# Optimization experiments

Hardware: AMD Instinct MI355X
Metric: run time of the kernel (lower is better)

## Reference

```python
import jax, jax.numpy as jnp
import numpy as np

N = 50000   # nodes
E = 800000  # edges (avg degree 16)
D = 128     # input = hidden = embedding dim
K1 = 25000  # ceil(0.5 * N)
K2 = 12500  # ceil(0.5 * K1)
LABELS = 5
BN_EPS = 1e-5


def _sage(x, src, dst, W, b, normalize):
    # old-PyG SAGEConv: remove self loops, add self loop, mean aggregate, linear, L2-normalize
    n = x.shape[0]
    dst_e = jnp.where(src == dst, n, dst)  # drop self loops; dummy edges (src=dst=n) also land in segment n
    s = jax.ops.segment_sum(x[src], dst_e, num_segments=n + 1)[:n]          # [n, d]
    deg = jax.ops.segment_sum(jnp.ones(src.shape, x.dtype), dst_e, num_segments=n + 1)[:n]
    agg = (s + x) / (deg + 1.0)[:, None]  # mean over neighbors + self
    out = agg @ W + b
    if normalize:
        out = out / jnp.maximum(jnp.linalg.norm(out, axis=-1, keepdims=True), 1e-12)
    return out


def _bn(x, g, b):
    # training-mode BatchNorm1d over nodes (biased variance, like torch)
    m = x.mean(axis=0)
    v = jnp.var(x, axis=0)
    return (x - m) / jnp.sqrt(v + BN_EPS) * g + b


def _sag_pool(x, src, dst, wp, bp, k):
    # SAGPooling: score = tanh(SAGEConv(x)->1), global top_k (single graph), filter_adj via dummy remap
    n = x.shape[0]
    score = jnp.tanh(_sage(x, src, dst, wp[:, None], bp, normalize=False)[:, 0])  # [n]
    score_k, perm = jax.lax.top_k(score, k)
    x2 = x[perm] * score_k[:, None]
    rank = jnp.full((n + 1,), -1, jnp.int32).at[perm].set(jnp.arange(k, dtype=jnp.int32))
    rs, rd = rank[src], rank[dst]
    valid = (rs >= 0) & (rd >= 0)
    src2 = jnp.where(valid, rs, k)  # invalid edges -> dummy node k
    dst2 = jnp.where(valid, rd, k)
    return x2, src2, dst2


def _forward(x, edge_index, Wc, bc, gamma, beta, Wpool, bpool, W1, b1, W2, b2):
    src, dst = edge_index[0], edge_index[1]
    # source bug replicated: stage 3 layer 2 uses bn_3_1's params
    bn_idx = [[0, 1, 2], [3, 4, 5], [6, 6, 8]]
    ks = [K1, K2]
    outs = []
    for s in range(3):
        for i in range(3):
            li = 3 * s + i
            x = jax.nn.relu(_sage(x, src, dst, Wc[li], bc[li], True))
            bi = bn_idx[s][i]
            x = _bn(x, gamma[bi], beta[bi])
        outs.append(jnp.max(x, axis=0))  # scatter_max with a single graph
        if s < 2:
            x, src, dst = _sag_pool(x, src, dst, Wpool[s], bpool[s], ks[s])
    h = jnp.concatenate(outs)[None, :]          # [1, 3*D]
    h = jax.nn.relu(h @ W1 + b1)
    return h @ W2 + b2                           # [1, LABELS]


def setup_inputs() -> dict:
    key = jax.random.key(0)
    ks = jax.random.split(key, 8)
    x = jax.random.normal(ks[0], (N, D), dtype=jnp.float32)
    edge_index = jax.random.randint(ks[1], (2, E), 0, N, dtype=jnp.int32)
    Wc = jax.random.normal(ks[2], (9, D, D), dtype=jnp.float32) / np.sqrt(D)
    bc = jnp.zeros((9, D), jnp.float32)
    gamma = jnp.ones((9, D), jnp.float32)
    beta = jnp.zeros((9, D), jnp.float32)
    Wpool = jax.random.normal(ks[3], (2, D), dtype=jnp.float32) / np.sqrt(D)
    bpool = jnp.zeros((2,), jnp.float32)
    W1 = jax.random.normal(ks[4], (3 * D, 50), dtype=jnp.float32) / np.sqrt(3 * D)
    b1 = jnp.zeros((50,), jnp.float32)
    W2 = jax.random.normal(ks[5], (50, LABELS), dtype=jnp.float32) / np.sqrt(50)
    b2 = jnp.zeros((LABELS,), jnp.float32)
    return {"x": x, "edge_index": edge_index, "Wc": Wc, "bc": bc, "gamma": gamma,
            "beta": beta, "Wpool": Wpool, "bpool": bpool,
            "W1": W1, "b1": b1, "W2": W2, "b2": b2}


def reference(x, edge_index, Wc, bc, gamma, beta, Wpool, bpool, W1, b1, W2, b2):
    return _forward(x, edge_index, Wc, bc, gamma, beta, Wpool, bpool, W1, b1, W2, b2)
```

## Files before the change

kernel.cpp:

```cpp
#include <hip/hip_runtime.h>

constexpr int FD   = 128;
constexpr int NMAX = 50000;
constexpr int EDG  = 800000;

static __device__ __forceinline__ unsigned enc(float f){
  unsigned u = __float_as_uint(f);
  return (u & 0x80000000u) ? ~u : (u | 0x80000000u);
}
static __device__ __forceinline__ float dec(unsigned e){
  unsigned u = (e & 0x80000000u) ? (e ^ 0x80000000u) : ~e;
  return __uint_as_float(u);
}

__global__ void k_count(const int* __restrict__ src, const int* __restrict__ dst,
                        int* __restrict__ deg, int E){
  int e = blockIdx.x*256 + threadIdx.x;
  if (e >= E) return;
  int s = src[e], d = dst[e];
  if (s != d) atomicAdd(&deg[d], 1);
}

__global__ void k_remap_count(const int* __restrict__ sIn, const int* __restrict__ dIn,
                              int* __restrict__ sOut, int* __restrict__ dOut,
                              const int* __restrict__ rank, int kNew,
                              int* __restrict__ deg, int E){
  int e = blockIdx.x*256 + threadIdx.x;
  if (e >= E) return;
  int s = sIn[e], d = dIn[e];
  int rs = rank[s], rd = rank[d];
  bool ok = (rs >= 0) && (rd >= 0);
  int os = ok ? rs : kNew, od = ok ? rd : kNew;
  sOut[e] = os; dOut[e] = od;
  if (os != od) atomicAdd(&deg[od], 1);
}

__global__ void k_scan(int* __restrict__ off, int* __restrict__ cur, int n){
  __shared__ int wsum[16];
  __shared__ int carry;
  int tid = threadIdx.x, lane = tid & 63, wid = tid >> 6;
  if (tid == 0) carry = 0;
  __syncthreads();
  for (int base = 0; base < n; base += 1024){
    int v = base + tid;
    int x = (v < n) ? off[v] : 0;
    int val = x;
    #pragma unroll
    for (int o = 1; o < 64; o <<= 1){ int t = __shfl_up(val, o); if (lane >= o) val += t; }
    if (lane == 63) wsum[wid] = val;
    __syncthreads();
    if (tid < 16){
      int v2 = wsum[tid];
      #pragma unroll
      for (int o = 1; o < 16; o <<= 1){ int t = __shfl_up(v2, o); if (tid >= o) v2 += t; }
      wsum[tid] = v2;
    }
    __syncthreads();
    int add = (wid > 0) ? wsum[wid-1] : 0;
    int incl = val + add;
    int c0 = carry;
    if (v < n){ int e0 = c0 + incl - x; off[v] = e0; cur[v] = e0; }
    __syncthreads();
    if (tid == 0) carry = c0 + wsum[15];
    __syncthreads();
  }
  if (tid == 0) off[n] = carry;
}

__global__ void k_fill(const int* __restrict__ src, const int* __restrict__ dst,
                       int* __restrict__ cur, int* __restrict__ csr, int E){
  int e = blockIdx.x*256 + threadIdx.x;
  if (e >= E) return;
  int s = src[e], d = dst[e];
  if (s != d){ int pos = atomicAdd(&cur[d], 1); csr[pos] = s; }
}

__global__ __launch_bounds__(256) void k_agg(const float* __restrict__ X,
    const int* __restrict__ off, const int* __restrict__ csr,
    float* __restrict__ AGG, int n,
    const float* __restrict__ st, const float* __restrict__ g,
    const float* __restrict__ bt, float invn){
  int tid = threadIdx.x;
  int v = blockIdx.x*4 + (tid >> 6);
  if (v >= n) return;
  int lane = tid & 63;
  int c = lane * 2;
  float ax = 1.f, ay = 1.f, bx = 0.f, by = 0.f;
  if (st){
    float ma = st[c]*invn, mb = st[c+1]*invn;
    float va = st[FD+c]*invn - ma*ma, vb = st[FD+c+1]*invn - mb*mb;
    ax = g[c]*rsqrtf(va + 1e-5f);  ay = g[c+1]*rsqrtf(vb + 1e-5f);
    bx = bt[c] - ma*ax;            by = bt[c+1] - mb*ay;
  }
  int b = off[v], e = off[v+1];
  int deg = e - b;
  float2 s = *(const float2*)(X + (size_t)v*FD + c);
  int j = 0;
  while (j < deg){
    int cnt = deg - j; if (cnt > 64) cnt = 64;
    int myu = (j + lane < deg) ? csr[b + j + lane] : 0;
    int t = 0;
    for (; t + 4 <= cnt; t += 4){
      int u0 = __shfl(myu, t);
      int u1 = __shfl(myu, t+1);
      int u2 = __shfl(myu, t+2);
      int u3 = __shfl(myu, t+3);
      float2 t0 = *(const float2*)(X + (size_t)u0*FD + c);
      float2 t1 = *(const float2*)(X + (size_t)u1*FD + c);
      float2 t2 = *(const float2*)(X + (size_t)u2*FD + c);
      float2 t3 = *(const float2*)(X + (size_t)u3*FD + c);
      s.x += t0.x + t1.x + t2.x + t3.x;
      s.y += t0.y + t1.y + t2.y + t3.y;
    }
    for (; t < cnt; t++){
      int u = __shfl(myu, t);
      float2 tt = *(const float2*)(X + (size_t)u*FD + c);
      s.x += tt.x; s.y += tt.y;
    }
    j += cnt;
  }
  float inv = 1.f / (float)(deg + 1);
  float2 o;
  o.x = s.x*inv*ax + bx;
  o.y = s.y*inv*ay + by;
  *(float2*)(AGG + (size_t)v*FD + c) = o;
}

__global__ __launch_bounds__(256,2) void k_gemm(const float* __restrict__ A,
    const float* __restrict__ W, const float* __restrict__ bias,
    float* __restrict__ Y, float* __restrict__ stats, int n,
    unsigned* __restrict__ cmx, unsigned* __restrict__ cmn){
  __shared__ float sW[FD*FD];
  __shared__ float ss[4][FD];
  __shared__ float sq_[4][FD];
  __shared__ float smx[4][FD];
  __shared__ float smn[4][FD];
  int tid = threadIdx.x;
  {
    const float4* Wg = (const float4*)W; float4* Ws = (float4*)sW;
    for (int i = tid; i < FD*FD/4; i += 256) Ws[i] = Wg[i];
  }
  __syncthreads();
  int tc = tid & 15;
  int tr = tid >> 4;
  int rbase = blockIdx.x*FD + tr*8;
  float acc[8][8];
  #pragma unroll
  for (int i = 0; i < 8; i++)
    #pragma unroll
    for (int j = 0; j < 8; j++) acc[i][j] = 0.f;

  for (int k4 = 0; k4 < FD; k4 += 4){
    float4 a[8];
    #pragma unroll
    for (int i = 0; i < 8; i++){
      int r = rbase + i; if (r >= n) r = n - 1;
      a[i] = *(const float4*)(A + (size_t)r*FD + k4);
    }
    #pragma unroll
    for (int kk = 0; kk < 4; kk++){
      const float* wr = &sW[(k4+kk)*FD + tc*8];
      float4 w0 = *(const float4*)wr, w1 = *(const float4*)(wr+4);
      #pragma unroll
      for (int i = 0; i < 8; i++){
        float av = (kk==0) ? a[i].x : (kk==1) ? a[i].y : (kk==2) ? a[i].z : a[i].w;
        acc[i][0] += av*w0.x; acc[i][1] += av*w0.y; acc[i][2] += av*w0.z; acc[i][3] += av*w0.w;
        acc[i][4] += av*w1.x; acc[i][5] += av*w1.y; acc[i][6] += av*w1.z; acc[i][7] += av*w1.w;
      }
    }
  }
  float bx[8];
  {
    const float* bp = bias + tc*8;
    #pragma unroll
    for (int j = 0; j < 8; j++) bx[j] = bp[j];
  }
  float cs[8], cq[8], mxv[8], mnv[8];
  #pragma unroll
  for (int j = 0; j < 8; j++){ cs[j]=0.f; cq[j]=0.f; mxv[j]=-3.4e38f; mnv[j]=3.4e38f; }
  #pragma unroll
  for (int i = 0; i < 8; i++){
    int r = rbase + i;
    bool valid = (r < n);
    float y[8]; float sq = 0.f;
    #pragma unroll
    for (int j = 0; j < 8; j++){ y[j] = acc[i][j] + bx[j]; sq += y[j]*y[j]; }
    sq += __shfl_xor(sq,1); sq += __shfl_xor(sq,2); sq += __shfl_xor(sq,4); sq += __shfl_xor(sq,8);
    float nrm = sqrtf(sq);
    float sc = 1.f / fmaxf(nrm, 1e-12f);
    #pragma unroll
    for (int j = 0; j < 8; j++){ y[j] *= sc; y[j] = fmaxf(y[j], 0.f); }
    if (valid){
      float* yo = Y + (size_t)r*FD + tc*8;
      *(float4*)yo     = make_float4(y[0],y[1],y[2],y[3]);
      *(float4*)(yo+4) = make_float4(y[4],y[5],y[6],y[7]);
      #pragma unroll
      for (int j = 0; j < 8; j++){
        cs[j] += y[j]; cq[j] += y[j]*y[j];
        mxv[j] = fmaxf(mxv[j], y[j]); mnv[j] = fminf(mnv[j], y[j]);
      }
    }
  }
  #pragma unroll
  for (int j = 0; j < 8; j++){
    cs[j] += __shfl_xor(cs[j],16); cs[j] += __shfl_xor(cs[j],32);
    cq[j] += __shfl_xor(cq[j],16); cq[j] += __shfl_xor(cq[j],32);
    mxv[j] = fmaxf(mxv[j], __shfl_xor(mxv[j],16)); mxv[j] = fmaxf(mxv[j], __shfl_xor(mxv[j],32));
    mnv[j] = fminf(mnv[j], __shfl_xor(mnv[j],16)); mnv[j] = fminf(mnv[j], __shfl_xor(mnv[j],32));
  }
  int wv = tid >> 6, lane = tid & 63;
  if (lane < 16){
    #pragma unroll
    for (int j = 0; j < 8; j++){
      ss[wv][tc*8+j] = cs[j]; sq_[wv][tc*8+j] = cq[j];
      smx[wv][tc*8+j] = mxv[j]; smn[wv][tc*8+j] = mnv[j];
    }
  }
  __syncthreads();
  if (tid < FD){
    float s_ = ss[0][tid]+ss[1][tid]+ss[2][tid]+ss[3][tid];
    float q_ = sq_[0][tid]+sq_[1][tid]+sq_[2][tid]+sq_[3][tid];
    atomicAdd(&stats[tid], s_);
    atomicAdd(&stats[FD+tid], q_);
    if (cmx){
      float mx = fmaxf(fmaxf(smx[0][tid],smx[1][tid]), fmaxf(smx[2][tid],smx[3][tid]));
      float mn = fminf(fminf(smn[0][tid],smn[1][tid]), fminf(smn[2][tid],smn[3][tid]));
      atomicMax(&cmx[tid], enc(mx));
      atomicMin(&cmn[tid], enc(mn));
    }
  }
}

__global__ __launch_bounds__(256) void k_dotp(const float* __restrict__ X,
    const float* __restrict__ wp,
    const float* __restrict__ st, const float* __restrict__ g,
    const float* __restrict__ bt, float invn,
    float* __restrict__ p, int n){
  int tid = threadIdx.x;
  int v = blockIdx.x*4 + (tid >> 6), lane = tid & 63;
  if (v >= n) return;
  int c = lane * 2;
  float ma = st[c]*invn, mb = st[c+1]*invn;
  float va = st[FD+c]*invn - ma*ma, vb = st[FD+c+1]*invn - mb*mb;
  float ax = g[c]*rsqrtf(va + 1e-5f), ay = g[c+1]*rsqrtf(vb + 1e-5f);
  float bx = bt[c] - ma*ax,           by = bt[c+1] - mb*ay;
  float2 x = *(const float2*)(X + (size_t)v*FD + c);
  float2 w = *(const float2*)(wp + c);
  float s = (ax*x.x + bx)*w.x + (ay*x.y + by)*w.y;
  s += __shfl_xor(s,1); s += __shfl_xor(s,2); s += __shfl_xor(s,4);
  s += __shfl_xor(s,8); s += __shfl_xor(s,16); s += __shfl_xor(s,32);
  if (lane == 0) p[v] = s;
}

__global__ void k_score(const float* __restrict__ p, const int* __restrict__ off,
    const int* __restrict__ csr, const float* __restrict__ bpool, int pi,
    float* __restrict__ score, int n){
  int v = blockIdx.x*256 + threadIdx.x;
  if (v >= n) return;
  int b = off[v], e = off[v+1];
  float s = p[v];
  for (int j = b; j < e; j++) s += p[csr[j]];
  score[v] = tanhf(s / (float)(e - b + 1) + bpool[pi]);
}

__global__ void k_hist_hi(const float* __restrict__ score, int n, unsigned* __restrict__ hist){
  int v = blockIdx.x*256 + threadIdx.x;
  if (v >= n) return;
  unsigned key = enc(score[v]);
  atomicAdd(&hist[key >> 16], 1u);
}

__global__ void k_hist_lo(const float* __restrict__ score, int n,
                          const unsigned* __restrict__ state, unsigned* __restrict__ hist){
  int v = blockIdx.x*256 + threadIdx.x;
  if (v >= n) return;
  unsigned key = enc(score[v]);
  if ((key >> 16) == state[5]) atomicAdd(&hist[key & 0xFFFFu], 1u);
}

__global__ __launch_bounds__(1024) void k_pick(const unsigned* __restrict__ hist,
                                               unsigned* __restrict__ state, int k, int pass){
  __shared__ unsigned wsum[16];
  int tid = threadIdx.x;
  unsigned want = (pass == 0) ? (unsigned)k : state[4];
  unsigned prevAbove = (pass == 0) ? 0u : state[1];
  int chunk = 1023 - tid;
  const unsigned* hbase = hist + chunk*64;
  unsigned csum = 0;
  #pragma unroll
  for (int j = 0; j < 64; j++) csum += hbase[j];
  unsigned val = csum;
  int lane = tid & 63, wid = tid >> 6;
  #pragma unroll
  for (int o = 1; o < 64; o <<= 1){ unsigned t = __shfl_up(val, o); if (lane >= o) val += t; }
  if (lane == 63) wsum[wid] = val;
  __syncthreads();
  if (tid < 16){
    unsigned v2 = wsum[tid];
    #pragma unroll
    for (int o = 1; o < 16; o <<= 1){ unsigned t = __shfl_up(v2, o); if (tid >= o) v2 += t; }
    wsum[tid] = v2;
  }
  __syncthreads();
  unsigned incl = val + ((wid > 0) ? wsum[wid-1] : 0u);
  unsigned excl = incl - csum;
  if (excl < want && incl >= want){
    unsigned cum = excl, above = 0; int bsel = 0;
    for (int j = 63; j >= 0; j--){
      unsigned cc = hbase[j];
      if (cum + cc >= want){ bsel = j; above = cum; break; }
      cum += cc;
    }
    unsigned bucket = (unsigned)(chunk*64 + bsel);
    if (pass == 0){
      state[5] = bucket;
      state[1] = prevAbove + above;
      state[4] = want - above;
    } else {
      unsigned T = (state[5] << 16) | bucket;
      unsigned totAbove = prevAbove + above;
      state[0] = T; state[1] = totAbove; state[2] = 0u; state[3] = totAbove;
    }
  }
}

__global__ void k_compact(const float* __restrict__ score, unsigned* __restrict__ state,
    int* __restrict__ rank, int* __restrict__ sel, int n, int k){
  int v = blockIdx.x*256 + threadIdx.x;
  if (v > n) return;
  if (v == n){ rank[n] = -1; return; }
  unsigned T = state[0];
  unsigned key = enc(score[v]);
  int slot = -1;
  if (key > T) slot = (int)atomicAdd(&state[2], 1u);
  else if (key == T){ unsigned t = atomicAdd(&state[3], 1u); if (t < (unsigned)k) slot = (int)t; }
  rank[v] = slot;
  if (slot >= 0) sel[slot] = v;
}

__global__ __launch_bounds__(256) void k_gather(const float* __restrict__ X,
    const int* __restrict__ sel, const float* __restrict__ score,
    const float* __restrict__ st, const float* __restrict__ g,
    const float* __restrict__ bt, float invn,
    float* __restrict__ XO, int k){
  int j = blockIdx.x*4 + (threadIdx.x >> 6), lane = threadIdx.x & 63;
  if (j >= k) return;
  int c = lane * 2;
  float ma = st[c]*invn, mb = st[c+1]*invn;
  float va = st[FD+c]*invn - ma*ma, vb = st[FD+c+1]*invn - mb*mb;
  float ax = g[c]*rsqrtf(va + 1e-5f), ay = g[c+1]*rsqrtf(vb + 1e-5f);
  float bx = bt[c] - ma*ax,           by = bt[c+1] - mb*ay;
  int u = sel[j];
  float sc = score[u];
  float2 t = *(const float2*)(X + (size_t)u*FD + c);
  t.x = (ax*t.x + bx)*sc; t.y = (ay*t.y + by)*sc;
  *(float2*)(XO + (size_t)j*FD + c) = t;
}

__global__ void k_final(const unsigned* __restrict__ cmx, const unsigned* __restrict__ cmn,
    const float* __restrict__ stats, const float* __restrict__ gamma,
    const float* __restrict__ beta,
    const float* __restrict__ W1, const float* __restrict__ b1,
    const float* __restrict__ W2, const float* __restrict__ b2,
    float* __restrict__ out){
  __shared__ float h[384];
  __shared__ float h1[50];
  int tid = threadIdx.x;
  if (tid < 384){
    int s = tid >> 7, c = tid & 127;
    const int liR[3] = {2,5,8};
    const float nsf[3] = {50000.f, 25000.f, 12500.f};
    int li = liR[s];
    const float* st = stats + (size_t)li*256;
    float invn = 1.f / nsf[s];
    float m = st[c]*invn, vv = st[FD+c]*invn - m*m;
    float a = gamma[(size_t)li*FD+c]*rsqrtf(vv + 1e-5f);
    float bb = beta[(size_t)li*FD+c] - m*a;
    float mx = dec(cmx[tid]), mn = dec(cmn[tid]);
    h[tid] = (a >= 0.f) ? (a*mx + bb) : (a*mn + bb);
  }
  __syncthreads();
  if (tid < 50){
    float acc = b1[tid];
    for (int i = 0; i < 384; i++) acc += h[i]*W1[i*50 + tid];
    h1[tid] = fmaxf(acc, 0.f);
  }
  __syncthreads();
  if (tid < 5){
    float acc = b2[tid];
    for (int i = 0; i < 50; i++) acc += h1[i]*W2[i*5 + tid];
    out[tid] = acc;
  }
}

extern "C" void kernel_launch(void* const* d_in, const int* in_sizes, int n_in,
                              void* d_out, int out_size, void* d_ws, size_t ws_size,
                              hipStream_t stream){
  (void)in_sizes; (void)n_in; (void)out_size; (void)ws_size;
  const float* x_in  = (const float*)d_in[0];
  const int*   ei    = (const int*)d_in[1];
  const float* Wc    = (const float*)d_in[2];
  const float* bc    = (const float*)d_in[3];
  const float* gamma = (const float*)d_in[4];
  const float* beta  = (const float*)d_in[5];
  const float* Wpool = (const float*)d_in[6];
  const float* bpool = (const float*)d_in[7];
  const float* W1    = (const float*)d_in[8];
  const float* b1    = (const float*)d_in[9];
  const float* W2    = (const float*)d_in[10];
  const float* b2    = (const float*)d_in[11];
  float* dout = (float*)d_out;

  char* base = (char*)d_ws; size_t o_ = 0;
  auto alloc = [&](size_t bytes)->void*{
    void* p = base + o_; o_ = (o_ + bytes + 255) & ~(size_t)255; return p;
  };
  float* B0   = (float*)alloc((size_t)NMAX*FD*4);
  float* B1   = (float*)alloc((size_t)NMAX*FD*4);
  int* eSrc   = (int*)alloc((size_t)EDG*4);
  int* eDst   = (int*)alloc((size_t)EDG*4);
  int* offv   = (int*)alloc((size_t)(NMAX+1)*4);
  int* cur    = (int*)alloc((size_t)NMAX*4);
  int* csr    = (int*)alloc((size_t)EDG*4);
  float* pbuf = (float*)alloc((size_t)NMAX*4);
  float* sbuf = (float*)alloc((size_t)NMAX*4);
  int* sel    = (int*)alloc((size_t)25000*4);
  int* rank   = (int*)alloc((size_t)(NMAX+1)*4);
  float* stats= (float*)alloc(9*256*4);
  unsigned* cmx = (unsigned*)alloc(384*4);
  unsigned* cmn = (unsigned*)alloc(384*4);
  unsigned* state= (unsigned*)alloc(64);
  unsigned* hist = (unsigned*)alloc(2*65536*4);

  const int ns[3]  = {50000, 25000, 12500};
  const int bnIdx[9] = {0,1,2,3,4,5,6,6,8};
  const int EB = (EDG + 255)/256;

  hipMemsetAsync(stats, 0, 9*256*4, stream);
  hipMemsetAsync(cmx, 0x00, 384*4, stream);
  hipMemsetAsync(cmn, 0xFF, 384*4, stream);

  const int* cs = ei;
  const int* cd = ei + EDG;

  for (int s = 0; s < 3; s++){
    int n = ns[s];
    float fin = 1.f/(float)n;
    float* X = (s == 1) ? B1 : B0;
    float* A = (s == 1) ? B0 : B1;

    hipMemsetAsync(offv, 0, (size_t)(n+1)*4, stream);
    if (s == 0){
      k_count<<<dim3(EB), dim3(256), 0, stream>>>(cs, cd, offv, EDG);
    } else {
      k_remap_count<<<dim3(EB), dim3(256), 0, stream>>>(cs, cd, eSrc, eDst, rank, n, offv, EDG);
      cs = eSrc; cd = eDst;
    }
    k_scan<<<1, 1024, 0, stream>>>(offv, cur, n);
    k_fill<<<dim3(EB), dim3(256), 0, stream>>>(cs, cd, cur, csr, EDG);

    for (int i = 0; i < 3; i++){
      int li = s*3 + i;
      const float* xr = (s == 0 && i == 0) ? x_in : (const float*)X;
      const float* stPrev = (i == 0) ? (const float*)nullptr : stats + (size_t)(li-1)*256;
      int gb = (i == 0) ? 0 : bnIdx[li-1];
      bool rd = (i == 2);
      k_agg<<<dim3((n+3)/4), dim3(256), 0, stream>>>(xr, offv, csr, A, n,
                                                     stPrev, gamma + (size_t)gb*FD, beta + (size_t)gb*FD, fin);
      k_gemm<<<dim3((n+FD-1)/FD), dim3(256), 0, stream>>>(A, Wc + (size_t)li*FD*FD, bc + li*FD, X,
                                                          stats + (size_t)li*256, n,
                                                          rd ? (cmx + s*FD) : (unsigned*)nullptr,
                                                          rd ? (cmn + s*FD) : (unsigned*)nullptr);
    }

    if (s < 2){
      int k = (s == 0) ? 25000 : 12500;
      int li2 = s*3 + 2;
      const float* st2 = stats + (size_t)li2*256;
      const float* g2 = gamma + (size_t)bnIdx[li2]*FD;
      const float* bt2 = beta + (size_t)bnIdx[li2]*FD;
      k_dotp<<<dim3((n+3)/4), dim3(256), 0, stream>>>(X, Wpool + s*FD, st2, g2, bt2, fin, pbuf, n);
      k_score<<<dim3((n+255)/256), dim3(256), 0, stream>>>(pbuf, offv, csr, bpool, s, sbuf, n);
      hipMemsetAsync(hist, 0, 2*65536*4, stream);
      k_hist_hi<<<dim3((n+255)/256), dim3(256), 0, stream>>>(sbuf, n, hist);
      k_pick<<<1, 1024, 0, stream>>>(hist, state, k, 0);
      k_hist_lo<<<dim3((n+255)/256), dim3(256), 0, stream>>>(sbuf, n, state, hist + 65536);
      k_pick<<<1, 1024, 0, stream>>>(hist + 65536, state, k, 1);
      k_compact<<<dim3((n+256)/256), dim3(256), 0, stream>>>(sbuf, state, rank, sel, n, k);
      k_gather<<<dim3((k+3)/4), dim3(256), 0, stream>>>(X, sel, sbuf, st2, g2, bt2, fin, A, k);
    }
  }
  k_final<<<1, 384, 0, stream>>>(cmx, cmn, stats, gamma, beta, W1, b1, W2, b2, dout);
}
```

Baseline: 1.043 ms.

## Parallelize CSR offset scan with atomics, fuse histogram into score, unroll gather

Replaces the single-block serial scan with a multi-block scan. Each block takes its base offset from an atomic counter, so CSR segments end up in arbitrary block order, and aggregation now reads a start array plus the degree instead of adjacent offsets. The high-bit histogram pass is folded into the score kernel, and the neighbor gather loop is unrolled to eight loads. The aim is to remove a long single-block serial kernel, save one launch, and expose more memory-level parallelism, at the cost of extra register pressure and a non-deterministic segment layout.

```diff
diff --git a/kernel.cpp b/kernel.cpp
--- a/kernel.cpp
+++ b/kernel.cpp
@@ -35,36 +35,26 @@
   if (os != od) atomicAdd(&deg[od], 1);
 }
 
-__global__ void k_scan(int* __restrict__ off, int* __restrict__ cur, int n){
-  __shared__ int wsum[16];
-  __shared__ int carry;
+__global__ __launch_bounds__(256) void k_offsets(const int* __restrict__ deg,
+    int* __restrict__ start, int* __restrict__ cur, int* __restrict__ total, int n){
+  __shared__ int wsum[4];
+  __shared__ int sbase;
   int tid = threadIdx.x, lane = tid & 63, wid = tid >> 6;
-  if (tid == 0) carry = 0;
-  __syncthreads();
-  for (int base = 0; base < n; base += 1024){
-    int v = base + tid;
-    int x = (v < n) ? off[v] : 0;
-    int val = x;
-    #pragma unroll
-    for (int o = 1; o < 64; o <<= 1){ int t = __shfl_up(val, o); if (lane >= o) val += t; }
-    if (lane == 63) wsum[wid] = val;
-    __syncthreads();
-    if (tid < 16){
-      int v2 = wsum[tid];
-      #pragma unroll
-      for (int o = 1; o < 16; o <<= 1){ int t = __shfl_up(v2, o); if (tid >= o) v2 += t; }
-      wsum[tid] = v2;
-    }
-    __syncthreads();
-    int add = (wid > 0) ? wsum[wid-1] : 0;
-    int incl = val + add;
-    int c0 = carry;
-    if (v < n){ int e0 = c0 + incl - x; off[v] = e0; cur[v] = e0; }
-    __syncthreads();
-    if (tid == 0) carry = c0 + wsum[15];
-    __syncthreads();
-  }
-  if (tid == 0) off[n] = carry;
+  int v = blockIdx.x*256 + tid;
+  int x = (v < n) ? deg[v] : 0;
+  int val = x;
+  #pragma unroll
+  for (int o = 1; o < 64; o <<= 1){ int t = __shfl_up(val, o); if (lane >= o) val += t; }
+  if (lane == 63) wsum[wid] = val;
+  __syncthreads();
+  if (tid == 0){
+    int t0 = wsum[0], t1 = wsum[1], t2 = wsum[2], t3 = wsum[3];
+    sbase = atomicAdd(total, t0+t1+t2+t3);
+    wsum[0] = 0; wsum[1] = t0; wsum[2] = t0+t1; wsum[3] = t0+t1+t2;
+  }
+  __syncthreads();
+  int excl = (val - x) + wsum[wid] + sbase;
+  if (v < n){ start[v] = excl; cur[v] = excl; }
 }
 
 __global__ void k_fill(const int* __restrict__ src, const int* __restrict__ dst,
@@ -76,7 +66,8 @@
 }
 
 __global__ __launch_bounds__(256) void k_agg(const float* __restrict__ X,
-    const int* __restrict__ off, const int* __restrict__ csr,
+    const int* __restrict__ start, const int* __restrict__ degb,
+    const int* __restrict__ csr,
     float* __restrict__ AGG, int n,
     const float* __restrict__ st, const float* __restrict__ g,
     const float* __restrict__ bt, float invn){
@@ -92,25 +83,39 @@
     ax = g[c]*rsqrtf(va + 1e-5f);  ay = g[c+1]*rsqrtf(vb + 1e-5f);
     bx = bt[c] - ma*ax;            by = bt[c+1] - mb*ay;
   }
-  int b = off[v], e = off[v+1];
-  int deg = e - b;
+  int b = start[v];
+  int deg = degb[v];
   float2 s = *(const float2*)(X + (size_t)v*FD + c);
   int j = 0;
   while (j < deg){
     int cnt = deg - j; if (cnt > 64) cnt = 64;
     int myu = (j + lane < deg) ? csr[b + j + lane] : 0;
     int t = 0;
-    for (; t + 4 <= cnt; t += 4){
-      int u0 = __shfl(myu, t);
-      int u1 = __shfl(myu, t+1);
-      int u2 = __shfl(myu, t+2);
-      int u3 = __shfl(myu, t+3);
+    for (; t + 8 <= cnt; t += 8){
+      int u0 = __shfl(myu, t),   u1 = __shfl(myu, t+1);
+      int u2 = __shfl(myu, t+2), u3 = __shfl(myu, t+3);
+      int u4 = __shfl(myu, t+4), u5 = __shfl(myu, t+5);
+      int u6 = __shfl(myu, t+6), u7 = __shfl(myu, t+7);
       float2 t0 = *(const float2*)(X + (size_t)u0*FD + c);
       float2 t1 = *(const float2*)(X + (size_t)u1*FD + c);
       float2 t2 = *(const float2*)(X + (size_t)u2*FD + c);
       float2 t3 = *(const float2*)(X + (size_t)u3*FD + c);
-      s.x += t0.x + t1.x + t2.x + t3.x;
-      s.y += t0.y + t1.y + t2.y + t3.y;
+      float2 t4 = *(const float2*)(X + (size_t)u4*FD + c);
+      float2 t5 = *(const float2*)(X + (size_t)u5*FD + c);
+      float2 t6 = *(const float2*)(X + (size_t)u6*FD + c);
+      float2 t7 = *(const float2*)(X + (size_t)u7*FD + c);
+      s.x += ((t0.x + t1.x) + (t2.x + t3.x)) + ((t4.x + t5.x) + (t6.x + t7.x));
+      s.y += ((t0.y + t1.y) + (t2.y + t3.y)) + ((t4.y + t5.y) + (t6.y + t7.y));
+    }
+    for (; t + 4 <= cnt; t += 4){
+      int u0 = __shfl(myu, t),   u1 = __shfl(myu, t+1);
+      int u2 = __shfl(myu, t+2), u3 = __shfl(myu, t+3);
+      float2 t0 = *(const float2*)(X + (size_t)u0*FD + c);
+      float2 t1 = *(const float2*)(X + (size_t)u1*FD + c);
+      float2 t2 = *(const float2*)(X + (size_t)u2*FD + c);
+      float2 t3 = *(const float2*)(X + (size_t)u3*FD + c);
+      s.x += (t0.x + t1.x) + (t2.x + t3.x);
+      s.y += (t0.y + t1.y) + (t2.y + t3.y);
     }
     for (; t < cnt; t++){
       int u = __shfl(myu, t);
@@ -252,22 +257,18 @@
   if (lane == 0) p[v] = s;
 }
 
-__global__ void k_score(const float* __restrict__ p, const int* __restrict__ off,
-    const int* __restrict__ csr, const float* __restrict__ bpool, int pi,
-    float* __restrict__ score, int n){
+__global__ void k_score(const float* __restrict__ p, const int* __restrict__ start,
+    const int* __restrict__ degb, const int* __restrict__ csr,
+    const float* __restrict__ bpool, int pi,
+    float* __restrict__ score, unsigned* __restrict__ hist, int n){
   int v = blockIdx.x*256 + threadIdx.x;
   if (v >= n) return;
-  int b = off[v], e = off[v+1];
+  int b = start[v], deg = degb[v];
   float s = p[v];
-  for (int j = b; j < e; j++) s += p[csr[j]];
-  score[v] = tanhf(s / (float)(e - b + 1) + bpool[pi]);
-}
-
-__global__ void k_hist_hi(const float* __restrict__ score, int n, unsigned* __restrict__ hist){
-  int v = blockIdx.x*256 + threadIdx.x;
-  if (v >= n) return;
-  unsigned key = enc(score[v]);
-  atomicAdd(&hist[key >> 16], 1u);
+  for (int j = 0; j < deg; j++) s += p[csr[b+j]];
+  float sc = tanhf(s / (float)(deg + 1) + bpool[pi]);
+  score[v] = sc;
+  atomicAdd(&hist[enc(sc) >> 16], 1u);
 }
 
 __global__ void k_hist_lo(const float* __restrict__ score, int n,
@@ -419,7 +420,8 @@
   float* B1   = (float*)alloc((size_t)NMAX*FD*4);
   int* eSrc   = (int*)alloc((size_t)EDG*4);
   int* eDst   = (int*)alloc((size_t)EDG*4);
-  int* offv   = (int*)alloc((size_t)(NMAX+1)*4);
+  int* degb   = (int*)alloc((size_t)(NMAX+1)*4);
+  int* startv = (int*)alloc((size_t)NMAX*4);
   int* cur    = (int*)alloc((size_t)NMAX*4);
   int* csr    = (int*)alloc((size_t)EDG*4);
   float* pbuf = (float*)alloc((size_t)NMAX*4);
@@ -449,14 +451,14 @@
     float* X = (s == 1) ? B1 : B0;
     float* A = (s == 1) ? B0 : B1;
 
-    hipMemsetAsync(offv, 0, (size_t)(n+1)*4, stream);
+    hipMemsetAsync(degb, 0, (size_t)(n+1)*4, stream);
     if (s == 0){
-      k_count<<<dim3(EB), dim3(256), 0, stream>>>(cs, cd, offv, EDG);
+      k_count<<<dim3(EB), dim3(256), 0, stream>>>(cs, cd, degb, EDG);
     } else {
-      k_remap_count<<<dim3(EB), dim3(256), 0, stream>>>(cs, cd, eSrc, eDst, rank, n, offv, EDG);
+      k_remap_count<<<dim3(EB), dim3(256), 0, stream>>>(cs, cd, eSrc, eDst, rank, n, degb, EDG);
       cs = eSrc; cd = eDst;
     }
-    k_scan<<<1, 1024, 0, stream>>>(offv, cur, n);
+    k_offsets<<<dim3((n+255)/256), dim3(256), 0, stream>>>(degb, startv, cur, degb + n, n);
     k_fill<<<dim3(EB), dim3(256), 0, stream>>>(cs, cd, cur, csr, EDG);
 
     for (int i = 0; i < 3; i++){
@@ -465,7 +467,7 @@
       const float* stPrev = (i == 0) ? (const float*)nullptr : stats + (size_t)(li-1)*256;
       int gb = (i == 0) ? 0 : bnIdx[li-1];
       bool rd = (i == 2);
-      k_agg<<<dim3((n+3)/4), dim3(256), 0, stream>>>(xr, offv, csr, A, n,
+      k_agg<<<dim3((n+3)/4), dim3(256), 0, stream>>>(xr, startv, degb, csr, A, n,
                                                      stPrev, gamma + (size_t)gb*FD, beta + (size_t)gb*FD, fin);
       k_gemm<<<dim3((n+FD-1)/FD), dim3(256), 0, stream>>>(A, Wc + (size_t)li*FD*FD, bc + li*FD, X,
                                                           stats + (size_t)li*256, n,
@@ -479,10 +481,9 @@
       const float* st2 = stats + (size_t)li2*256;
       const float* g2 = gamma + (size_t)bnIdx[li2]*FD;
       const float* bt2 = beta + (size_t)bnIdx[li2]*FD;
+      hipMemsetAsync(hist, 0, 2*65536*4, stream);
       k_dotp<<<dim3((n+3)/4), dim3(256), 0, stream>>>(X, Wpool + s*FD, st2, g2, bt2, fin, pbuf, n);
-      k_score<<<dim3((n+255)/256), dim3(256), 0, stream>>>(pbuf, offv, csr, bpool, s, sbuf, n);
-      hipMemsetAsync(hist, 0, 2*65536*4, stream);
-      k_hist_hi<<<dim3((n+255)/256), dim3(256), 0, stream>>>(sbuf, n, hist);
+      k_score<<<dim3((n+255)/256), dim3(256), 0, stream>>>(pbuf, startv, degb, csr, bpool, s, sbuf, hist, n);
       k_pick<<<1, 1024, 0, stream>>>(hist, state, k, 0);
       k_hist_lo<<<dim3((n+255)/256), dim3(256), 0, stream>>>(sbuf, n, state, hist + 65536);
       k_pick<<<1, 1024, 0, stream>>>(hist + 65536, state, k, 1);
```

Result: faster. 962.3 us (-7.7%).
